# Optimization experiments

Hardware: AMD Instinct MI355X
Metric: run time of the kernel (lower is better)

The kernel has to match this reference:

```python
import jax, jax.numpy as jnp
import numpy as np

B, T, D, H = 1024, 128, 128, 256

def _uni(k, shape, fan):
    s = 1.0 / np.sqrt(fan)
    return jax.random.uniform(k, shape, jnp.float32, -s, s)

def setup_inputs():
    key = jax.random.key(0)
    ks = jax.random.split(key, 22)
    inp = {}
    inp['x'] = jax.random.normal(ks[0], (B, T, D), jnp.float32)
    inp['x_hat'] = jax.random.normal(ks[1], (B, T, D), jnp.float32)
    inp['u'] = jax.random.uniform(ks[2], (B, T, D), jnp.float32)
    inp['m'] = (jax.random.uniform(ks[3], (B, T, D)) < 0.8).astype(jnp.float32)
    inp['d'] = jax.random.uniform(ks[4], (B, T, D), jnp.float32)
    # Decay(D -> H)
    inp['W_decay'] = _uni(ks[5], (H, D), D)
    inp['b_decay'] = _uni(ks[6], (H,), D)
    # hist: Linear(H -> D)
    inp['W_hist'] = _uni(ks[7], (D, H), H)
    inp['b_hist'] = _uni(ks[8], (D,), H)
    inp['Wv'] = _uni(ks[9], (D, D), D)
    inp['bv'] = _uni(ks[10], (D,), D)
    inp['Wr'] = _uni(ks[11], (D, D), D)
    inp['br'] = _uni(ks[12], (D,), D)
    # Conv1d(2,1,kernel=1) == learned 2-way combine
    inp['conv_w'] = _uni(ks[13], (2,), 2)
    inp['conv_b'] = _uni(ks[14], (), 2)
    # GRUCell(2*D -> H), torch layout [3H, in] rows = (r, z, n)
    inp['W_ih'] = _uni(ks[15], (3 * H, 2 * D), 2 * D)
    inp['W_hh'] = _uni(ks[16], (3 * H, H), H)
    inp['b_ih'] = _uni(ks[17], (3 * H,), H)
    inp['b_hh'] = _uni(ks[18], (3 * H,), H)
    # fc_out: Linear(H -> 1)
    inp['W_out'] = _uni(ks[19], (1, H), H)
    inp['b_out'] = _uni(ks[20], (1,), H)
    return inp

def reference(x, x_hat, u, m, d, W_decay, b_decay, W_hist, b_hist, Wv, bv, Wr, br,
              conv_w, conv_b, W_ih, W_hh, b_ih, b_hh, W_out, b_out):
    off = 1.0 - jnp.eye(D, dtype=x.dtype)
    # Precompute everything that does not depend on the recurrent state h:
    gamma = jnp.exp(-jax.nn.relu(jnp.einsum('btd,hd->bth', d, W_decay) + b_decay))  # [B,T,H]
    xbar = m * x + (1.0 - m) * x_hat
    xu = jnp.einsum('btd,ed->bte', xbar, Wv * off) + bv  # [B,T,D] (unc_flag == 0 path)
    Wr_m = Wr * off

    def step(carry, inp):
        h, loss = carry
        x_t, m_t, g_t, xu_t = inp  # [B,D],[B,D],[B,H],[B,D]
        h = h * g_t
        x_h = h @ W_hist.T + b_hist
        x_r = m_t * x_t + (1.0 - m_t) * x_h
        xr = x_r @ Wr_m.T + br
        x_comb = conv_w[0] * xu_t + conv_w[1] * xr + conv_b  # Conv1d(2,1,1)
        loss = loss + jnp.sum(jnp.abs(x_t - x_comb) * m_t) / (jnp.sum(m_t) + 1e-5)
        x_imp = m_t * x_t + (1.0 - m_t) * x_comb
        gin = jnp.concatenate([x_imp, m_t], axis=1)  # [B, 2D]
        gi = gin @ W_ih.T + b_ih
        gh = h @ W_hh.T + b_hh
        i_r, i_z, i_n = jnp.split(gi, 3, axis=1)
        h_r, h_z, h_n = jnp.split(gh, 3, axis=1)
        r = jax.nn.sigmoid(i_r + h_r)
        z = jax.nn.sigmoid(i_z + h_z)
        n = jnp.tanh(i_n + r * h_n)
        h_new = (1.0 - z) * n + z * h
        return (h_new, loss), (x_imp, xr)

    h0 = jnp.zeros((B, H), x.dtype)
    xs = (jnp.swapaxes(x, 0, 1), jnp.swapaxes(m, 0, 1),
          jnp.swapaxes(gamma, 0, 1), jnp.swapaxes(xu, 0, 1))
    (h_fin, x_loss), (x_imp_t, xr_t) = jax.lax.scan(step, (h0, jnp.float32(0.0)), xs)
    x_imp = jnp.swapaxes(x_imp_t, 0, 1)  # [B,T,D]
    xrs = jnp.swapaxes(xr_t, 0, 1)
    y_out = h_fin @ W_out.T + b_out  # task == 'C', get_y == True
    y_score = jax.nn.sigmoid(y_out)
    return (x_imp, y_out, y_score, x_loss, xu, xrs)
```

## Files before the change

kernel.cpp:

```cpp
#include <hip/hip_runtime.h>
#include <math.h>

#define BQ 1024
#define TT 128
#define DD 128
#define HH 256
#define NW 8
#define NTH 512
#define NBLK 64

typedef float f32x4 __attribute__((ext_vector_type(4)));
typedef __bf16 bf16x8 __attribute__((ext_vector_type(8)));
typedef unsigned short u16x4 __attribute__((ext_vector_type(4)));
typedef unsigned short u16x8 __attribute__((ext_vector_type(8)));
typedef unsigned int u32x4 __attribute__((ext_vector_type(4)));
typedef unsigned int u32x2 __attribute__((ext_vector_type(2)));
typedef long long i64;

#define WS_MSUMF 8192
#define WS_WQ8   40960
#define WS_WB16  487424
#define WS_SA1   589824
#define WS_SA2   67698688

#define TQ_TOT  864

#define TB_DEC 0
#define TB_WV  64
#define TB_TOT 96

#define L_WX  0
#define L_HI  98304
#define L_WR  131072
#define L_HF8 147456
#define L_XRF 151552
#define L_XIF 153600
#define L_RED 155648
#define L_TOT 155712

__device__ __forceinline__ unsigned short f2bf(float f){
  union { float f; unsigned u; } v; v.f = f;
  unsigned r = v.u + 0x7FFFu + ((v.u >> 16) & 1u);
  return (unsigned short)(r >> 16);
}
__device__ __forceinline__ float sigm(float v){ return 1.f/(1.f + __expf(-v)); }
__device__ __forceinline__ float tanhfast(float v){ return 2.f*sigm(2.f*v) - 1.f; }
__device__ __forceinline__ unsigned pk4(float a, float b, float c, float d){
  int v = __builtin_amdgcn_cvt_pk_fp8_f32(a, b, 0, false);
  v = __builtin_amdgcn_cvt_pk_fp8_f32(c, d, v, true);
  return (unsigned)v;
}
__device__ __forceinline__ f32x4 upk4(unsigned w){
  f32x4 r;
  r[0] = __builtin_amdgcn_cvt_f32_fp8((int)w, 0);
  r[1] = __builtin_amdgcn_cvt_f32_fp8((int)w, 1);
  r[2] = __builtin_amdgcn_cvt_f32_fp8((int)w, 2);
  r[3] = __builtin_amdgcn_cvt_f32_fp8((int)w, 3);
  return r;
}
__device__ __forceinline__ f32x4 mfma8(i64 a, i64 b, f32x4 c){
  return __builtin_amdgcn_mfma_f32_16x16x32_fp8_fp8(a, b, c, 0, 0, 0);
}
__device__ __forceinline__ f32x4 mfma16b(bf16x8 a, bf16x8 b, f32x4 c){
  return __builtin_amdgcn_mfma_f32_16x16x32_bf16(a, b, c, 0, 0, 0);
}

__global__ void pack_w8(const float* Whh, const float* Wih, const float* Whist,
                        const float* Wr, unsigned char* wq){
  int gt = blockIdx.x*4 + (threadIdx.x>>6);
  int lane = threadIdx.x & 63;
  if (gt >= TQ_TOT) return;
  int lr = lane & 15, lg = lane >> 4;
  const float* src; int n, k0, K; int dm = 0;
  if (gt < 384){ int kt = gt & 7, gnt = gt >> 3;
    n = (gnt>>4)*256 + (gnt&15)*16 + lr; k0 = kt*32 + lg*8; src = Whh; K = 256; }
  else if (gt < 576){ int id = gt-384; int kt = id & 3, gnt = id >> 2;
    n = (gnt>>4)*256 + (gnt&15)*16 + lr; k0 = kt*32 + lg*8; src = Wih; K = 256; }
  else if (gt < 640){ int id = gt-576; int kt = id & 7, nt = id >> 3;
    n = nt*16 + lr; k0 = kt*32 + lg*8; src = Whist; K = 256; }
  else if (gt < 672){ int id = gt-640; int kt = id & 3, nt = id >> 2;
    n = nt*16 + lr; k0 = kt*32 + lg*8; src = Wr; K = 128; dm = 1; }
  else { int id = gt-672; int kt = id & 3, gnt = id >> 2;
    n = (gnt>>4)*256 + (gnt&15)*16 + lr; k0 = 128 + kt*32 + lg*8; src = Wih; K = 256; }
  float f[8];
  #pragma unroll
  for (int e = 0; e < 8; ++e){
    int k = k0 + e;
    float v = src[(size_t)n*K + k];
    if (dm && n == k) v = 0.f;
    f[e] = v;
  }
  unsigned lo = pk4(f[0],f[1],f[2],f[3]), hi = pk4(f[4],f[5],f[6],f[7]);
  *(unsigned*)(wq + (size_t)gt*512 + lane*8) = lo;
  *(unsigned*)(wq + (size_t)gt*512 + lane*8 + 4) = hi;
}

__global__ void pack_w16(const float* Wdec, const float* Wv, unsigned short* wb){
  int gt = blockIdx.x*4 + (threadIdx.x>>6);
  int lane = threadIdx.x & 63;
  if (gt >= TB_TOT) return;
  int lr = lane & 15, lg = lane >> 4;
  const float* src; int n; int dm = 0; int kt;
  if (gt < TB_WV){ kt = gt & 3; n = (gt>>2)*16 + lr; src = Wdec; }
  else { int id = gt - TB_WV; kt = id & 3; n = (id>>2)*16 + lr; src = Wv; dm = 1; }
  int k0 = kt*32 + lg*8;
  u16x8 pkv;
  #pragma unroll
  for (int e = 0; e < 8; ++e){
    int k = k0 + e;
    float v = src[(size_t)n*128 + k];
    if (dm && n == k) v = 0.f;
    pkv[e] = f2bf(v);
  }
  *(u16x8*)(wb + (size_t)gt*512 + lane*8) = pkv;
}

__global__ void msum_kernel(const float* m, float* wsf){
  int t = blockIdx.x;
  float s = 0.f;
  for (int i = threadIdx.x; i < BQ*DD/4; i += 256){
    int b = i >> 5, c4 = (i & 31)*4;
    f32x4 v = *(const f32x4*)(m + ((size_t)b*TT + t)*DD + c4);
    s += v[0]+v[1]+v[2]+v[3];
  }
  #pragma unroll
  for (int off = 32; off >= 1; off >>= 1) s += __shfl_down(s, off);
  __shared__ float ps[4];
  if ((threadIdx.x & 63) == 0) ps[threadIdx.x >> 6] = s;
  __syncthreads();
  if (threadIdx.x == 0) wsf[WS_MSUMF + t] = ps[0] + ps[1] + ps[2] + ps[3];
}

__global__ void loss_final(const float* wsf, float* out_loss){
  __shared__ float ps[TT];
  int t = threadIdx.x;
  float s = 0.f;
  #pragma unroll 4
  for (int b = 0; b < NBLK; ++b) s += wsf[t*NBLK + b];
  ps[t] = s / (wsf[WS_MSUMF + t] + 1e-5f);
  __syncthreads();
  if (t == 0){ float a = 0.f; for (int i = 0; i < TT; ++i) a += ps[i]; *out_loss = a; }
}

__global__ __launch_bounds__(NTH, 2) void prep1_kernel(
    const float* __restrict__ x, const float* __restrict__ xhat,
    const float* __restrict__ m, const float* __restrict__ dly,
    const float* __restrict__ b_dec, const float* __restrict__ bv,
    const unsigned short* __restrict__ wb, unsigned* __restrict__ saA,
    float* __restrict__ out_xu)
{
  __shared__ __align__(16) char sm[12288];
  const int tid = threadIdx.x, w = tid>>6, lane = tid&63, lr = lane&15, lg = lane>>4;
  const int btile = blockIdx.x >> 4, tch = blockIdx.x & 15, b0 = btile*16;
  const int tg0 = tch*8;
  const int colD = w*16 + lr, colH0 = w*32 + lr;
  bf16x8 decR[2][4], wvR[4];
  #pragma unroll
  for (int s = 0; s < 2; ++s)
    #pragma unroll
    for (int kt = 0; kt < 4; ++kt)
      decR[s][kt] = *(const bf16x8*)(wb + (size_t)(TB_DEC + (w*2+s)*4 + kt)*512 + lane*8);
  #pragma unroll
  for (int kt = 0; kt < 4; ++kt)
    wvR[kt] = *(const bf16x8*)(wb + (size_t)(TB_WV + w*4 + kt)*512 + lane*8);
  const float bd0 = b_dec[colH0], bd1 = b_dec[colH0+16], bvv = bv[colD];
  const int srow = tid >> 5, c4 = (tid & 31)*4;
  const int kt_ = c4 >> 5, dl_ = ((c4 & 31) >> 3)*16 + srow, e0_ = c4 & 7;
  const size_t gbase = (size_t)(b0 + srow)*TT*DD + c4;

  f32x4 xv = *(const f32x4*)(x    + gbase + (size_t)tg0*DD);
  f32x4 hv = *(const f32x4*)(xhat + gbase + (size_t)tg0*DD);
  f32x4 mv = *(const f32x4*)(m    + gbase + (size_t)tg0*DD);
  f32x4 dv = *(const f32x4*)(dly  + gbase + (size_t)tg0*DD);

  for (int tt = 0; tt < 8; ++tt){
    int tg = tg0 + tt;
    u16x4 pd, pxb, pm;
    #pragma unroll
    for (int e = 0; e < 4; ++e){
      pd[e]  = f2bf(dv[e]);
      pxb[e] = f2bf(mv[e]*xv[e] + (1.f - mv[e])*hv[e]);
      pm[e]  = f2bf(mv[e]);
    }
    *(u16x4*)(sm + 0    + kt_*1024 + dl_*16 + e0_*2) = pd;
    *(u16x4*)(sm + 4096 + kt_*1024 + dl_*16 + e0_*2) = pxb;
    *(u16x4*)(sm + 8192 + srow*256 + c4*2) = pm;
    __syncthreads();

    {
      size_t g2 = gbase + (size_t)((tt < 7) ? tg+1 : tg)*DD;
      xv = *(const f32x4*)(x + g2);
      hv = *(const f32x4*)(xhat + g2);
      mv = *(const f32x4*)(m + g2);
      dv = *(const f32x4*)(dly + g2);
    }

    f32x4 ga0 = {0.f,0.f,0.f,0.f}, ga1 = {0.f,0.f,0.f,0.f}, xu4 = {0.f,0.f,0.f,0.f};
    #pragma unroll
    for (int kt = 0; kt < 4; ++kt){
      bf16x8 df  = *(const bf16x8*)(sm + 0    + kt*1024 + lane*16);
      bf16x8 xbf = *(const bf16x8*)(sm + 4096 + kt*1024 + lane*16);
      ga0 = mfma16b(df, decR[0][kt], ga0);
      ga1 = mfma16b(df, decR[1][kt], ga1);
      xu4 = mfma16b(xbf, wvR[kt], xu4);
    }
    float g0[4], g1[4], xuo[4];
    unsigned mask = 0;
    #pragma unroll
    for (int r = 0; r < 4; ++r){
      g0[r] = __expf(-fmaxf(ga0[r] + bd0, 0.f));
      g1[r] = __expf(-fmaxf(ga1[r] + bd1, 0.f));
      xuo[r] = xu4[r] + bvv;
      int row = lg*4 + r;
      unsigned short mu = *(const unsigned short*)(sm + 8192 + row*256 + colD*2);
      mask |= (mu ? 1u : 0u) << r;
    }
    u32x4 rec = {pk4(g0[0],g0[1],g0[2],g0[3]), pk4(g1[0],g1[1],g1[2],g1[3]),
                 pk4(xuo[0],xuo[1],xuo[2],xuo[3]), mask};
    __builtin_nontemporal_store(rec,
        (u32x4*)(saA + (((size_t)tg*NBLK + btile)*512 + tid)*4));
    #pragma unroll
    for (int r = 0; r < 4; ++r)
      __builtin_nontemporal_store(xuo[r], out_xu + ((size_t)(b0 + lg*4 + r)*TT + tg)*DD + colD);
    __syncthreads();
  }
}

__global__ __launch_bounds__(NTH, 2) void prep2_kernel(
    const float* __restrict__ m, const float* __restrict__ b_ih,
    const float* __restrict__ b_hh, const unsigned char* __restrict__ wq,
    unsigned* __restrict__ saB)
{
  __shared__ __align__(16) char sm[2048];
  const int tid = threadIdx.x, w = tid>>6, lane = tid&63, lr = lane&15, lg = lane>>4;
  const int btile = blockIdx.x >> 4, tch = blockIdx.x & 15, b0 = btile*16;
  const int tg0 = tch*8;
  i64 wihmR[6][4];
  float bfold[6];
  #pragma unroll
  for (int g = 0; g < 3; ++g)
    #pragma unroll
    for (int s = 0; s < 2; ++s){
      int j = g*2 + s;
      #pragma unroll
      for (int kt = 0; kt < 4; ++kt)
        wihmR[j][kt] = *(const i64*)(wq + (size_t)(672 + (g*16 + w*2+s)*4 + kt)*512 + lane*8);
      int n = g*256 + w*32 + s*16 + lr;
      bfold[j] = b_ih[n] + ((g < 2) ? b_hh[n] : 0.f);
    }
  const int srow = tid >> 5, c4 = (tid & 31)*4;
  const int kt_ = c4 >> 5, lg2 = (c4 & 31) >> 3, e0_ = c4 & 7;
  const size_t gbase = (size_t)(b0 + srow)*TT*DD + c4;

  for (int tt = 0; tt < 8; ++tt){
    int tg = tg0 + tt;
    f32x4 mv = *(const f32x4*)(m + gbase + (size_t)tg*DD);
    unsigned wbyte = 0;
    #pragma unroll
    for (int e = 0; e < 4; ++e) wbyte |= (mv[e] > 0.5f ? 0x38u : 0u) << (8*e);
    *(unsigned*)(sm + kt_*512 + (lg2*16 + srow)*8 + e0_) = wbyte;
    __syncthreads();

    i64 ma[4];
    #pragma unroll
    for (int kt = 0; kt < 4; ++kt) ma[kt] = *(const i64*)(sm + kt*512 + lane*8);
    f32x4 z4 = {0.f,0.f,0.f,0.f};
    f32x4 acc[6] = {z4,z4,z4,z4,z4,z4};
    #pragma unroll
    for (int j = 0; j < 6; ++j)
      #pragma unroll
      for (int kt = 0; kt < 4; ++kt)
        acc[j] = mfma8(ma[kt], wihmR[j][kt], acc[j]);
    unsigned wd[6];
    #pragma unroll
    for (int j = 0; j < 6; ++j)
      wd[j] = pk4(acc[j][0]+bfold[j], acc[j][1]+bfold[j], acc[j][2]+bfold[j], acc[j][3]+bfold[j]);
    unsigned* rp = saB + (((size_t)tg*NBLK + btile)*512 + tid)*6;
    u32x2 p0 = {wd[0], wd[1]}, p1 = {wd[2], wd[3]}, p2 = {wd[4], wd[5]};
    __builtin_nontemporal_store(p0, (u32x2*)rp);
    __builtin_nontemporal_store(p1, (u32x2*)(rp+2));
    __builtin_nontemporal_store(p2, (u32x2*)(rp+4));
    __syncthreads();
  }
}

__global__ __launch_bounds__(NTH) __attribute__((amdgpu_waves_per_eu(2, 2)))
void scan_kernel(
    const unsigned char* __restrict__ wq, const unsigned* __restrict__ saA,
    const unsigned* __restrict__ saB, const float* __restrict__ x,
    const float* __restrict__ b_hist, const float* __restrict__ br,
    const float* __restrict__ b_hh,
    const float* __restrict__ conv_w, const float* __restrict__ conv_b,
    const float* __restrict__ W_out, const float* __restrict__ b_out,
    float* __restrict__ lossP,
    float* __restrict__ out_ximp, float* __restrict__ out_y,
    float* __restrict__ out_ys, float* __restrict__ out_xrs)
{
  extern __shared__ __align__(16) char lds[];
  const int tid = threadIdx.x, w = tid>>6, lane = tid&63, lr = lane&15, lg = lane>>4;
  const int b0 = blockIdx.x*16;
  const int colD = w*16 + lr, colH0 = w*32 + lr;

  i64 whhR[3][2][8];
  #pragma unroll
  for (int g = 0; g < 3; ++g)
    #pragma unroll
    for (int s = 0; s < 2; ++s)
      #pragma unroll
      for (int kt = 0; kt < 8; ++kt)
        whhR[g][s][kt] = *(const i64*)(wq + (size_t)((g*16 + w*2+s)*8 + kt)*512 + lane*8);
  for (int i = tid; i < 9216; i += NTH)
    *(u32x4*)(lds + (size_t)i*16) = *(const u32x4*)(wq + (size_t)384*512 + (size_t)i*16);

  const float bhist_v = b_hist[colD], br_v = br[colD];
  const float bhhn0 = b_hh[512 + colH0], bhhn1 = b_hh[512 + colH0 + 16];
  const float cw0 = conv_w[0], cw1 = conv_w[1], cb = conv_b[0];

  const int hb0 = L_HF8 + w*512 + (lr>>3)*128 + lg*32 + (lr&7);
  const int f80 = (w>>1)*512 + ((w&1)*2 + (lr>>3))*128 + lg*32 + (lr&7);
  float* red = (float*)(lds + L_RED);

  float hs[2][4] = {{0.f,0.f,0.f,0.f},{0.f,0.f,0.f,0.f}};

  const unsigned* rpa = saA + ((size_t)blockIdx.x*512 + tid)*4;
  const unsigned* rpb = saB + ((size_t)blockIdx.x*512 + tid)*6;
  const size_t STA = (size_t)NBLK*512*4, STB = (size_t)NBLK*512*6;
  const float* xb = x + (size_t)(b0 + lg*4)*TT*DD + colD;

  u32x4 pfA = __builtin_nontemporal_load((const u32x4*)rpa);
  u32x2 pfB0 = __builtin_nontemporal_load((const u32x2*)rpb);
  u32x2 pfB1 = __builtin_nontemporal_load((const u32x2*)(rpb+2));
  u32x2 pfB2 = __builtin_nontemporal_load((const u32x2*)(rpb+4));
  float xc_[4];
  #pragma unroll
  for (int r = 0; r < 4; ++r) xc_[r] = xb[(size_t)r*TT*DD];

  #pragma unroll 1
  for (int t = 0; t < TT; ++t){
    const unsigned* npa = (t < TT-1) ? (rpa + STA) : rpa;
    const unsigned* npb = (t < TT-1) ? (rpb + STB) : rpb;
    int tn = (t < TT-1) ? t+1 : t;
    u32x4 nA = __builtin_nontemporal_load((const u32x4*)npa);
    u32x2 nB0 = __builtin_nontemporal_load((const u32x2*)npb);
    u32x2 nB1 = __builtin_nontemporal_load((const u32x2*)(npb+2));
    u32x2 nB2 = __builtin_nontemporal_load((const u32x2*)(npb+4));
    float xn_[4];
    #pragma unroll
    for (int r = 0; r < 4; ++r) xn_[r] = xb[(size_t)r*TT*DD + (size_t)tn*DD];

    {
      f32x4 gA0 = upk4(pfA[0]), gA1 = upk4(pfA[1]);
      #pragma unroll
      for (int r = 0; r < 4; ++r){
        hs[0][r] *= gA0[r];
        hs[1][r] *= gA1[r];
      }
    }
    unsigned q0 = pk4(hs[0][0], hs[0][1], hs[0][2], hs[0][3]);
    unsigned q1 = pk4(hs[1][0], hs[1][1], hs[1][2], hs[1][3]);
    #pragma unroll
    for (int r = 0; r < 4; ++r){
      *(unsigned char*)(lds + hb0 +       r*8) = (unsigned char)(q0 >> (8*r));
      *(unsigned char*)(lds + hb0 + 256 + r*8) = (unsigned char)(q1 >> (8*r));
    }
    __syncthreads();

    i64 ha[8];
    #pragma unroll
    for (int kt = 0; kt < 8; ++kt)
      ha[kt] = *(const i64*)(lds + L_HF8 + kt*512 + lane*8);
    f32x4 z4 = {0.f,0.f,0.f,0.f};
    f32x4 aRZ[2][2] = {{z4,z4},{z4,z4}};
    f32x4 aNh[2] = {z4,z4}, aNi[2] = {z4,z4}, xh4 = z4;
    #pragma unroll
    for (int s = 0; s < 2; ++s)
      #pragma unroll
      for (int kt = 0; kt < 8; ++kt){
        aRZ[0][s] = mfma8(ha[kt], whhR[0][s][kt], aRZ[0][s]);
        aRZ[1][s] = mfma8(ha[kt], whhR[1][s][kt], aRZ[1][s]);
        aNh[s]    = mfma8(ha[kt], whhR[2][s][kt], aNh[s]);
      }
    #pragma unroll
    for (int kt = 0; kt < 8; ++kt)
      xh4 = mfma8(ha[kt], *(const i64*)(lds + L_HI + (w*8+kt)*512 + lane*8), xh4);
    {
      unsigned mk = pfA[3];
      float x0 = (mk & 1u) ? xc_[0] : (xh4[0] + bhist_v);
      float x1 = (mk & 2u) ? xc_[1] : (xh4[1] + bhist_v);
      float x2 = (mk & 4u) ? xc_[2] : (xh4[2] + bhist_v);
      float x3 = (mk & 8u) ? xc_[3] : (xh4[3] + bhist_v);
      unsigned p = pk4(x0, x1, x2, x3);
      #pragma unroll
      for (int r = 0; r < 4; ++r)
        *(unsigned char*)(lds + L_XRF + f80 + r*8) = (unsigned char)((p >> (8*r)) & 0xff);
    }
    __syncthreads();

    f32x4 xr4 = z4;
    #pragma unroll
    for (int kt = 0; kt < 4; ++kt)
      xr4 = mfma8(*(const i64*)(lds + L_XRF + kt*512 + lane*8),
                  *(const i64*)(lds + L_WR + (w*4+kt)*512 + lane*8), xr4);
    float lpart = 0.f, xi_[4];
    unsigned mk = pfA[3];
    f32x4 xu4v = upk4(pfA[2]);
    #pragma unroll
    for (int r = 0; r < 4; ++r){
      int row = lg*4 + r;
      size_t go = ((size_t)(b0+row)*TT + t)*DD + colD;
      float xrv = xr4[r] + br_v;
      float xuv = xu4v[r];
      __builtin_nontemporal_store(xrv, out_xrs + go);
      float xc = cw0*xuv + cw1*xrv + cb;
      bool mb = (mk >> r) & 1u;
      lpart += mb ? fabsf(xc_[r] - xc) : 0.f;
      xi_[r] = mb ? xc_[r] : xc;
      __builtin_nontemporal_store(xi_[r], out_ximp + go);
    }
    {
      unsigned q = pk4(xi_[0], xi_[1], xi_[2], xi_[3]);
      #pragma unroll
      for (int r = 0; r < 4; ++r)
        *(unsigned char*)(lds + L_XIF + f80 + r*8) = (unsigned char)((q >> (8*r)) & 0xff);
    }
    #pragma unroll
    for (int off = 32; off >= 1; off >>= 1) lpart += __shfl_down(lpart, off);
    if (lane == 0) red[w] = lpart;
    __syncthreads();

    i64 xia[4];
    #pragma unroll
    for (int kt = 0; kt < 4; ++kt) xia[kt] = *(const i64*)(lds + L_XIF + kt*512 + lane*8);
    #pragma unroll
    for (int s = 0; s < 2; ++s)
      #pragma unroll
      for (int kt = 0; kt < 4; ++kt){
        aRZ[0][s] = mfma8(xia[kt], *(const i64*)(lds + L_WX + ((0*16 + w*2+s)*4 + kt)*512 + lane*8), aRZ[0][s]);
        aRZ[1][s] = mfma8(xia[kt], *(const i64*)(lds + L_WX + ((1*16 + w*2+s)*4 + kt)*512 + lane*8), aRZ[1][s]);
        aNi[s]    = mfma8(xia[kt], *(const i64*)(lds + L_WX + ((2*16 + w*2+s)*4 + kt)*512 + lane*8), aNi[s]);
      }
    if (tid == 0){
      float ssum = 0.f;
      #pragma unroll
      for (int i = 0; i < 8; ++i) ssum += red[i];
      lossP[t*NBLK + blockIdx.x] = ssum;
    }
    {
      f32x4 gR0 = upk4(pfB0[0]), gR1 = upk4(pfB0[1]);
      f32x4 gZ0 = upk4(pfB1[0]), gZ1 = upk4(pfB1[1]);
      f32x4 gN0 = upk4(pfB2[0]), gN1 = upk4(pfB2[1]);
      #pragma unroll
      for (int r = 0; r < 4; ++r){
        float rr0 = sigm(aRZ[0][0][r] + gR0[r]);
        float zz0 = sigm(aRZ[1][0][r] + gZ0[r]);
        float nn0 = tanhfast(aNi[0][r] + gN0[r] + rr0*(aNh[0][r] + bhhn0));
        hs[0][r] = (1.f - zz0)*nn0 + zz0*hs[0][r];
        float rr1 = sigm(aRZ[0][1][r] + gR1[r]);
        float zz1 = sigm(aRZ[1][1][r] + gZ1[r]);
        float nn1 = tanhfast(aNi[1][r] + gN1[r] + rr1*(aNh[1][r] + bhhn1));
        hs[1][r] = (1.f - zz1)*nn1 + zz1*hs[1][r];
      }
    }
    pfA = nA; pfB0 = nB0; pfB1 = nB1; pfB2 = nB2;
    xc_[0] = xn_[0]; xc_[1] = xn_[1]; xc_[2] = xn_[2]; xc_[3] = xn_[3];
    rpa = npa; rpb = npb;
  }

  __syncthreads();
  float* hfin = (float*)lds;
  #pragma unroll
  for (int s = 0; s < 2; ++s)
    #pragma unroll
    for (int r = 0; r < 4; ++r)
      hfin[(lg*4+r)*HH + colH0 + s*16] = hs[s][r];
  __syncthreads();
  float* psum = (float*)(lds + 16384);
  if (tid < 256){
    int row = tid >> 4, seg = tid & 15;
    float p = 0.f;
    #pragma unroll
    for (int c = 0; c < 16; ++c) p += hfin[row*HH + seg*16 + c]*W_out[seg*16 + c];
    psum[tid] = p;
  }
  __syncthreads();
  if (tid < 16){
    float yv = b_out[0];
    #pragma unroll
    for (int i = 0; i < 16; ++i) yv += psum[tid*16 + i];
    out_y[b0 + tid] = yv;
    out_ys[b0 + tid] = sigm(yv);
  }
}

extern "C" void kernel_launch(void* const* d_in, const int* in_sizes, int n_in,
                              void* d_out, int out_size, void* d_ws, size_t ws_size,
                              hipStream_t stream){
  const float* x     = (const float*)d_in[0];
  const float* xhat  = (const float*)d_in[1];
  const float* m     = (const float*)d_in[3];
  const float* dly   = (const float*)d_in[4];
  const float* Wdec  = (const float*)d_in[5];
  const float* b_dec = (const float*)d_in[6];
  const float* Whist = (const float*)d_in[7];
  const float* b_hist= (const float*)d_in[8];
  const float* Wv    = (const float*)d_in[9];
  const float* bvv   = (const float*)d_in[10];
  const float* Wr    = (const float*)d_in[11];
  const float* brr   = (const float*)d_in[12];
  const float* convw = (const float*)d_in[13];
  const float* convb = (const float*)d_in[14];
  const float* Wih   = (const float*)d_in[15];
  const float* Whh   = (const float*)d_in[16];
  const float* b_ih  = (const float*)d_in[17];
  const float* b_hh  = (const float*)d_in[18];
  const float* W_out = (const float*)d_in[19];
  const float* b_out = (const float*)d_in[20];

  float* wsf = (float*)d_ws;
  unsigned char* wq = (unsigned char*)d_ws + WS_WQ8;
  unsigned short* wb = (unsigned short*)((char*)d_ws + WS_WB16);
  unsigned* saA = (unsigned*)((char*)d_ws + WS_SA1);
  unsigned* saB = (unsigned*)((char*)d_ws + WS_SA2);

  float* out = (float*)d_out;
  size_t btd = (size_t)BQ*TT*DD;
  float* out_ximp = out;
  float* out_y    = out + btd;
  float* out_ys   = out_y + BQ;
  float* out_loss = out_ys + BQ;
  float* out_xu   = out_loss + 1;
  float* out_xrs  = out_xu + btd;

  (void)hipFuncSetAttribute((const void*)scan_kernel,
                            hipFuncAttributeMaxDynamicSharedMemorySize, L_TOT);

  pack_w8<<<TQ_TOT/4, 256, 0, stream>>>(Whh, Wih, Whist, Wr, wq);
  pack_w16<<<TB_TOT/4, 256, 0, stream>>>(Wdec, Wv, wb);
  msum_kernel<<<TT, 256, 0, stream>>>(m, wsf);
  prep1_kernel<<<1024, NTH, 0, stream>>>(x, xhat, m, dly, b_dec, bvv, wb, saA, out_xu);
  prep2_kernel<<<1024, NTH, 0, stream>>>(m, b_ih, b_hh, wq, saB);
  scan_kernel<<<NBLK, NTH, L_TOT, stream>>>(wq, saA, saB, x, b_hist, brr, b_hh,
      convw, convb, W_out, b_out, wsf,
      out_ximp, out_y, out_ys, out_xrs);
  loss_final<<<1, TT, 0, stream>>>(wsf, out_loss);
}
```

Baseline: 625.2 us.

## Fuse prep kernels and widen scan to 16 waves with split roles

```diff
diff --git a/kernel.cpp b/kernel.cpp
--- a/kernel.cpp
+++ b/kernel.cpp
@@ -5,8 +5,7 @@
 #define TT 128
 #define DD 128
 #define HH 256
-#define NW 8
-#define NTH 512
+#define NTH 1024
 #define NBLK 64
 
 typedef float f32x4 __attribute__((ext_vector_type(4)));
@@ -20,11 +19,11 @@
 #define WS_MSUMF 8192
 #define WS_WQ8   40960
 #define WS_WB16  487424
-#define WS_SA1   589824
-#define WS_SA2   67698688
+#define WS_SAG   589824
+#define WS_SAXM  34144256
+#define WS_SAB3  67698688
 
 #define TQ_TOT  864
-
 #define TB_DEC 0
 #define TB_WV  64
 #define TB_TOT 96
@@ -35,8 +34,9 @@
 #define L_HF8 147456
 #define L_XRF 151552
 #define L_XIF 153600
-#define L_RED 155648
-#define L_TOT 155712
+#define L_IMS 155648
+#define L_RED 156160
+#define L_TOT 156224
 
 __device__ __forceinline__ unsigned short f2bf(float f){
   union { float f; unsigned u; } v; v.f = f;
@@ -128,28 +128,26 @@
   __shared__ float ps[4];
   if ((threadIdx.x & 63) == 0) ps[threadIdx.x >> 6] = s;
   __syncthreads();
-  if (threadIdx.x == 0) wsf[WS_MSUMF + t] = ps[0] + ps[1] + ps[2] + ps[3];
-}
-
-__global__ void loss_final(const float* wsf, float* out_loss){
-  __shared__ float ps[TT];
-  int t = threadIdx.x;
-  float s = 0.f;
-  #pragma unroll 4
-  for (int b = 0; b < NBLK; ++b) s += wsf[t*NBLK + b];
-  ps[t] = s / (wsf[WS_MSUMF + t] + 1e-5f);
-  __syncthreads();
-  if (t == 0){ float a = 0.f; for (int i = 0; i < TT; ++i) a += ps[i]; *out_loss = a; }
-}
-
-__global__ __launch_bounds__(NTH, 2) void prep1_kernel(
+  if (threadIdx.x == 0) wsf[WS_MSUMF + t] = 1.f/(ps[0]+ps[1]+ps[2]+ps[3] + 1e-5f);
+}
+
+__global__ void loss_final(const float* lossP, float* out_loss){
+  float v = lossP[threadIdx.x];
+  #pragma unroll
+  for (int off = 32; off >= 1; off >>= 1) v += __shfl_down(v, off);
+  if (threadIdx.x == 0) *out_loss = v;
+}
+
+__global__ __launch_bounds__(512, 2) void prep_kernel(
     const float* __restrict__ x, const float* __restrict__ xhat,
     const float* __restrict__ m, const float* __restrict__ dly,
     const float* __restrict__ b_dec, const float* __restrict__ bv,
-    const unsigned short* __restrict__ wb, unsigned* __restrict__ saA,
-    float* __restrict__ out_xu)
+    const float* __restrict__ b_ih, const float* __restrict__ b_hh,
+    const unsigned short* __restrict__ wb, const unsigned char* __restrict__ wq,
+    unsigned* __restrict__ saG, unsigned* __restrict__ saXM,
+    unsigned* __restrict__ saB3, float* __restrict__ out_xu)
 {
-  __shared__ __align__(16) char sm[12288];
+  __shared__ __align__(16) char sm[14336];
   const int tid = threadIdx.x, w = tid>>6, lane = tid&63, lr = lane&15, lg = lane>>4;
   const int btile = blockIdx.x >> 4, tch = blockIdx.x & 15, b0 = btile*16;
   const int tg0 = tch*8;
@@ -163,6 +161,19 @@
   #pragma unroll
   for (int kt = 0; kt < 4; ++kt)
     wvR[kt] = *(const bf16x8*)(wb + (size_t)(TB_WV + w*4 + kt)*512 + lane*8);
+  i64 wihmR[6][4];
+  float bfold[6];
+  #pragma unroll
+  for (int g = 0; g < 3; ++g)
+    #pragma unroll
+    for (int s = 0; s < 2; ++s){
+      int j = g*2 + s;
+      #pragma unroll
+      for (int kt = 0; kt < 4; ++kt)
+        wihmR[j][kt] = *(const i64*)(wq + (size_t)(672 + (g*16 + w*2+s)*4 + kt)*512 + lane*8);
+      int n = g*256 + w*32 + s*16 + lr;
+      bfold[j] = b_ih[n] + ((g < 2) ? b_hh[n] : 0.f);
+    }
   const float bd0 = b_dec[colH0], bd1 = b_dec[colH0+16], bvv = bv[colD];
   const int srow = tid >> 5, c4 = (tid & 31)*4;
   const int kt_ = c4 >> 5, dl_ = ((c4 & 31) >> 3)*16 + srow, e0_ = c4 & 7;
@@ -176,15 +187,18 @@
   for (int tt = 0; tt < 8; ++tt){
     int tg = tg0 + tt;
     u16x4 pd, pxb, pm;
+    unsigned wbyte = 0;
     #pragma unroll
     for (int e = 0; e < 4; ++e){
       pd[e]  = f2bf(dv[e]);
       pxb[e] = f2bf(mv[e]*xv[e] + (1.f - mv[e])*hv[e]);
       pm[e]  = f2bf(mv[e]);
-    }
-    *(u16x4*)(sm + 0    + kt_*1024 + dl_*16 + e0_*2) = pd;
-    *(u16x4*)(sm + 4096 + kt_*1024 + dl_*16 + e0_*2) = pxb;
-    *(u16x4*)(sm + 8192 + srow*256 + c4*2) = pm;
+      wbyte |= (mv[e] > 0.5f ? 0x38u : 0u) << (8*e);
+    }
+    *(u16x4*)(sm + 0     + kt_*1024 + dl_*16 + e0_*2) = pd;
+    *(u16x4*)(sm + 4096  + kt_*1024 + dl_*16 + e0_*2) = pxb;
+    *(u16x4*)(sm + 8192  + srow*256 + c4*2) = pm;
+    *(unsigned*)(sm + 12288 + kt_*512 + dl_*8 + e0_) = wbyte;
     __syncthreads();
 
     {
@@ -195,7 +209,8 @@
       dv = *(const f32x4*)(dly + g2);
     }
 
-    f32x4 ga0 = {0.f,0.f,0.f,0.f}, ga1 = {0.f,0.f,0.f,0.f}, xu4 = {0.f,0.f,0.f,0.f};
+    f32x4 z4 = {0.f,0.f,0.f,0.f};
+    f32x4 ga0 = z4, ga1 = z4, xu4 = z4;
     #pragma unroll
     for (int kt = 0; kt < 4; ++kt){
       bf16x8 df  = *(const bf16x8*)(sm + 0    + kt*1024 + lane*16);
@@ -204,6 +219,16 @@
       ga1 = mfma16b(df, decR[1][kt], ga1);
       xu4 = mfma16b(xbf, wvR[kt], xu4);
     }
+    i64 ma[4];
+    #pragma unroll
+    for (int kt = 0; kt < 4; ++kt) ma[kt] = *(const i64*)(sm + 12288 + kt*512 + lane*8);
+    f32x4 acc[6] = {z4,z4,z4,z4,z4,z4};
+    #pragma unroll
+    for (int j = 0; j < 6; ++j)
+      #pragma unroll
+      for (int kt = 0; kt < 4; ++kt)
+        acc[j] = mfma8(ma[kt], wihmR[j][kt], acc[j]);
+
     float g0[4], g1[4], xuo[4];
     unsigned mask = 0;
     #pragma unroll
@@ -215,10 +240,25 @@
       unsigned short mu = *(const unsigned short*)(sm + 8192 + row*256 + colD*2);
       mask |= (mu ? 1u : 0u) << r;
     }
-    u32x4 rec = {pk4(g0[0],g0[1],g0[2],g0[3]), pk4(g1[0],g1[1],g1[2],g1[3]),
-                 pk4(xuo[0],xuo[1],xuo[2],xuo[3]), mask};
-    __builtin_nontemporal_store(rec,
-        (u32x4*)(saA + (((size_t)tg*NBLK + btile)*512 + tid)*4));
+    size_t base1024 = ((size_t)tg*NBLK + btile)*1024;
+    __builtin_nontemporal_store(pk4(g0[0],g0[1],g0[2],g0[3]),
+        saG + base1024 + (2*w+0)*64 + lane);
+    __builtin_nontemporal_store(pk4(g1[0],g1[1],g1[2],g1[3]),
+        saG + base1024 + (2*w+1)*64 + lane);
+    u32x2 xmrec = {pk4(xuo[0],xuo[1],xuo[2],xuo[3]), mask};
+    __builtin_nontemporal_store(xmrec,
+        (u32x2*)(saXM + (((size_t)tg*NBLK + btile)*512 + tid)*2));
+    #pragma unroll
+    for (int s = 0; s < 2; ++s){
+      size_t bb = (base1024 + (2*w+s)*64 + lane)*3;
+      #pragma unroll
+      for (int g = 0; g < 3; ++g){
+        f32x4 a = acc[g*2+s];
+        __builtin_nontemporal_store(
+            pk4(a[0]+bfold[g*2+s], a[1]+bfold[g*2+s], a[2]+bfold[g*2+s], a[3]+bfold[g*2+s]),
+            saB3 + bb + g);
+      }
+    }
     #pragma unroll
     for (int r = 0; r < 4; ++r)
       __builtin_nontemporal_store(xuo[r], out_xu + ((size_t)(b0 + lg*4 + r)*TT + tg)*DD + colD);
@@ -226,68 +266,11 @@
   }
 }
 
-__global__ __launch_bounds__(NTH, 2) void prep2_kernel(
-    const float* __restrict__ m, const float* __restrict__ b_ih,
-    const float* __restrict__ b_hh, const unsigned char* __restrict__ wq,
-    unsigned* __restrict__ saB)
-{
-  __shared__ __align__(16) char sm[2048];
-  const int tid = threadIdx.x, w = tid>>6, lane = tid&63, lr = lane&15, lg = lane>>4;
-  const int btile = blockIdx.x >> 4, tch = blockIdx.x & 15, b0 = btile*16;
-  const int tg0 = tch*8;
-  i64 wihmR[6][4];
-  float bfold[6];
-  #pragma unroll
-  for (int g = 0; g < 3; ++g)
-    #pragma unroll
-    for (int s = 0; s < 2; ++s){
-      int j = g*2 + s;
-      #pragma unroll
-      for (int kt = 0; kt < 4; ++kt)
-        wihmR[j][kt] = *(const i64*)(wq + (size_t)(672 + (g*16 + w*2+s)*4 + kt)*512 + lane*8);
-      int n = g*256 + w*32 + s*16 + lr;
-      bfold[j] = b_ih[n] + ((g < 2) ? b_hh[n] : 0.f);
-    }
-  const int srow = tid >> 5, c4 = (tid & 31)*4;
-  const int kt_ = c4 >> 5, lg2 = (c4 & 31) >> 3, e0_ = c4 & 7;
-  const size_t gbase = (size_t)(b0 + srow)*TT*DD + c4;
-
-  for (int tt = 0; tt < 8; ++tt){
-    int tg = tg0 + tt;
-    f32x4 mv = *(const f32x4*)(m + gbase + (size_t)tg*DD);
-    unsigned wbyte = 0;
-    #pragma unroll
-    for (int e = 0; e < 4; ++e) wbyte |= (mv[e] > 0.5f ? 0x38u : 0u) << (8*e);
-    *(unsigned*)(sm + kt_*512 + (lg2*16 + srow)*8 + e0_) = wbyte;
-    __syncthreads();
-
-    i64 ma[4];
-    #pragma unroll
-    for (int kt = 0; kt < 4; ++kt) ma[kt] = *(const i64*)(sm + kt*512 + lane*8);
-    f32x4 z4 = {0.f,0.f,0.f,0.f};
-    f32x4 acc[6] = {z4,z4,z4,z4,z4,z4};
-    #pragma unroll
-    for (int j = 0; j < 6; ++j)
-      #pragma unroll
-      for (int kt = 0; kt < 4; ++kt)
-        acc[j] = mfma8(ma[kt], wihmR[j][kt], acc[j]);
-    unsigned wd[6];
-    #pragma unroll
-    for (int j = 0; j < 6; ++j)
-      wd[j] = pk4(acc[j][0]+bfold[j], acc[j][1]+bfold[j], acc[j][2]+bfold[j], acc[j][3]+bfold[j]);
-    unsigned* rp = saB + (((size_t)tg*NBLK + btile)*512 + tid)*6;
-    u32x2 p0 = {wd[0], wd[1]}, p1 = {wd[2], wd[3]}, p2 = {wd[4], wd[5]};
-    __builtin_nontemporal_store(p0, (u32x2*)rp);
-    __builtin_nontemporal_store(p1, (u32x2*)(rp+2));
-    __builtin_nontemporal_store(p2, (u32x2*)(rp+4));
-    __syncthreads();
-  }
-}
-
-__global__ __launch_bounds__(NTH) __attribute__((amdgpu_waves_per_eu(2, 2)))
-void scan_kernel(
-    const unsigned char* __restrict__ wq, const unsigned* __restrict__ saA,
-    const unsigned* __restrict__ saB, const float* __restrict__ x,
+__global__ __launch_bounds__(NTH) void scan_kernel(
+    const unsigned char* __restrict__ wq,
+    const unsigned* __restrict__ saG, const unsigned* __restrict__ saXM,
+    const unsigned* __restrict__ saB3, const float* __restrict__ x,
+    const float* __restrict__ msumInv,
     const float* __restrict__ b_hist, const float* __restrict__ br,
     const float* __restrict__ b_hh,
     const float* __restrict__ conv_w, const float* __restrict__ conv_b,
@@ -299,92 +282,90 @@
   extern __shared__ __align__(16) char lds[];
   const int tid = threadIdx.x, w = tid>>6, lane = tid&63, lr = lane&15, lg = lane>>4;
   const int b0 = blockIdx.x*16;
-  const int colD = w*16 + lr, colH0 = w*32 + lr;
-
-  i64 whhR[3][2][8];
+  const int wD = w & 7;
+  const int colH = w*16 + lr;
+  const int colD = wD*16 + lr;
+  const bool isLo = (w < 8);
+
+  i64 whhR[3][8];
   #pragma unroll
   for (int g = 0; g < 3; ++g)
     #pragma unroll
-    for (int s = 0; s < 2; ++s)
-      #pragma unroll
-      for (int kt = 0; kt < 8; ++kt)
-        whhR[g][s][kt] = *(const i64*)(wq + (size_t)((g*16 + w*2+s)*8 + kt)*512 + lane*8);
+    for (int kt = 0; kt < 8; ++kt)
+      whhR[g][kt] = *(const i64*)(wq + (size_t)((g*16 + w)*8 + kt)*512 + lane*8);
   for (int i = tid; i < 9216; i += NTH)
     *(u32x4*)(lds + (size_t)i*16) = *(const u32x4*)(wq + (size_t)384*512 + (size_t)i*16);
+  if (tid < TT) *(float*)(lds + L_IMS + tid*4) = msumInv[tid];
 
   const float bhist_v = b_hist[colD], br_v = br[colD];
-  const float bhhn0 = b_hh[512 + colH0], bhhn1 = b_hh[512 + colH0 + 16];
+  const float bhhn = b_hh[512 + colH];
   const float cw0 = conv_w[0], cw1 = conv_w[1], cb = conv_b[0];
 
-  const int hb0 = L_HF8 + w*512 + (lr>>3)*128 + lg*32 + (lr&7);
-  const int f80 = (w>>1)*512 + ((w&1)*2 + (lr>>3))*128 + lg*32 + (lr&7);
-  float* red = (float*)(lds + L_RED);
-
-  float hs[2][4] = {{0.f,0.f,0.f,0.f},{0.f,0.f,0.f,0.f}};
-
-  const unsigned* rpa = saA + ((size_t)blockIdx.x*512 + tid)*4;
-  const unsigned* rpb = saB + ((size_t)blockIdx.x*512 + tid)*6;
-  const size_t STA = (size_t)NBLK*512*4, STB = (size_t)NBLK*512*6;
+  const int hb16 = L_HF8 + (w>>1)*512 + ((w&1)*2 + (lr>>3))*128 + lg*32 + (lr&7);
+  const int f80  = (wD>>1)*512 + ((wD&1)*2 + (lr>>3))*128 + lg*32 + (lr&7);
+
+  float hs[4] = {0.f,0.f,0.f,0.f};
+  float lacc = 0.f;
+
+  const unsigned* pGp  = saG + (size_t)blockIdx.x*1024 + tid;
+  const unsigned* pXMp = saXM + ((size_t)blockIdx.x*512 + wD*64 + lane)*2;
+  const unsigned* pB3p = saB3 + ((size_t)blockIdx.x*1024 + tid)*3;
   const float* xb = x + (size_t)(b0 + lg*4)*TT*DD + colD;
-
-  u32x4 pfA = __builtin_nontemporal_load((const u32x4*)rpa);
-  u32x2 pfB0 = __builtin_nontemporal_load((const u32x2*)rpb);
-  u32x2 pfB1 = __builtin_nontemporal_load((const u32x2*)(rpb+2));
-  u32x2 pfB2 = __builtin_nontemporal_load((const u32x2*)(rpb+4));
+  const size_t STG = (size_t)NBLK*1024, STXM = (size_t)NBLK*1024, STB3 = (size_t)NBLK*3072;
+
+  unsigned pG = __builtin_nontemporal_load(pGp);
+  u32x2 pXM = __builtin_nontemporal_load((const u32x2*)pXMp);
+  unsigned pR = __builtin_nontemporal_load(pB3p);
+  unsigned pZ = __builtin_nontemporal_load(pB3p+1);
+  unsigned pN = __builtin_nontemporal_load(pB3p+2);
   float xc_[4];
   #pragma unroll
   for (int r = 0; r < 4; ++r) xc_[r] = xb[(size_t)r*TT*DD];
+  __syncthreads();
 
   #pragma unroll 1
   for (int t = 0; t < TT; ++t){
-    const unsigned* npa = (t < TT-1) ? (rpa + STA) : rpa;
-    const unsigned* npb = (t < TT-1) ? (rpb + STB) : rpb;
+    const unsigned* nGp  = (t < TT-1) ? (pGp + STG) : pGp;
+    const unsigned* nXMp = (t < TT-1) ? (pXMp + STXM) : pXMp;
+    const unsigned* nB3p = (t < TT-1) ? (pB3p + STB3) : pB3p;
     int tn = (t < TT-1) ? t+1 : t;
-    u32x4 nA = __builtin_nontemporal_load((const u32x4*)npa);
-    u32x2 nB0 = __builtin_nontemporal_load((const u32x2*)npb);
-    u32x2 nB1 = __builtin_nontemporal_load((const u32x2*)(npb+2));
-    u32x2 nB2 = __builtin_nontemporal_load((const u32x2*)(npb+4));
+    unsigned nG = __builtin_nontemporal_load(nGp);
+    u32x2 nXM = __builtin_nontemporal_load((const u32x2*)nXMp);
+    unsigned nR = __builtin_nontemporal_load(nB3p);
+    unsigned nZ = __builtin_nontemporal_load(nB3p+1);
+    unsigned nN = __builtin_nontemporal_load(nB3p+2);
     float xn_[4];
     #pragma unroll
     for (int r = 0; r < 4; ++r) xn_[r] = xb[(size_t)r*TT*DD + (size_t)tn*DD];
 
     {
-      f32x4 gA0 = upk4(pfA[0]), gA1 = upk4(pfA[1]);
-      #pragma unroll
-      for (int r = 0; r < 4; ++r){
-        hs[0][r] *= gA0[r];
-        hs[1][r] *= gA1[r];
+      f32x4 g4 = upk4(pG);
+      #pragma unroll
+      for (int r = 0; r < 4; ++r) hs[r] *= g4[r];
+    }
+    unsigned q0 = pk4(hs[0], hs[1], hs[2], hs[3]);
+    #pragma unroll
+    for (int r = 0; r < 4; ++r)
+      *(unsigned char*)(lds + hb16 + r*8) = (unsigned char)(q0 >> (8*r));
+    __syncthreads();
+
+    f32x4 z4 = {0.f,0.f,0.f,0.f};
+    f32x4 aR = z4, aZ = z4, aNh = z4;
+    #pragma unroll
+    for (int kt = 0; kt < 8; ++kt){
+      i64 ha = *(const i64*)(lds + L_HF8 + kt*512 + lane*8);
+      aR  = mfma8(ha, whhR[0][kt], aR);
+      aZ  = mfma8(ha, whhR[1][kt], aZ);
+      aNh = mfma8(ha, whhR[2][kt], aNh);
+    }
+    if (!isLo){
+      f32x4 xh4 = z4;
+      #pragma unroll
+      for (int kt = 0; kt < 8; ++kt){
+        i64 ha = *(const i64*)(lds + L_HF8 + kt*512 + lane*8);
+        xh4 = mfma8(ha, *(const i64*)(lds + L_HI + (wD*8+kt)*512 + lane*8), xh4);
       }
-    }
-    unsigned q0 = pk4(hs[0][0], hs[0][1], hs[0][2], hs[0][3]);
-    unsigned q1 = pk4(hs[1][0], hs[1][1], hs[1][2], hs[1][3]);
-    #pragma unroll
-    for (int r = 0; r < 4; ++r){
-      *(unsigned char*)(lds + hb0 +       r*8) = (unsigned char)(q0 >> (8*r));
-      *(unsigned char*)(lds + hb0 + 256 + r*8) = (unsigned char)(q1 >> (8*r));
-    }
-    __syncthreads();
-
-    i64 ha[8];
-    #pragma unroll
-    for (int kt = 0; kt < 8; ++kt)
-      ha[kt] = *(const i64*)(lds + L_HF8 + kt*512 + lane*8);
-    f32x4 z4 = {0.f,0.f,0.f,0.f};
-    f32x4 aRZ[2][2] = {{z4,z4},{z4,z4}};
-    f32x4 aNh[2] = {z4,z4}, aNi[2] = {z4,z4}, xh4 = z4;
-    #pragma unroll
-    for (int s = 0; s < 2; ++s)
-      #pragma unroll
-      for (int kt = 0; kt < 8; ++kt){
-        aRZ[0][s] = mfma8(ha[kt], whhR[0][s][kt], aRZ[0][s]);
-        aRZ[1][s] = mfma8(ha[kt], whhR[1][s][kt], aRZ[1][s]);
-        aNh[s]    = mfma8(ha[kt], whhR[2][s][kt], aNh[s]);
-      }
-    #pragma unroll
-    for (int kt = 0; kt < 8; ++kt)
-      xh4 = mfma8(ha[kt], *(const i64*)(lds + L_HI + (w*8+kt)*512 + lane*8), xh4);
-    {
-      unsigned mk = pfA[3];
+      unsigned mk = pXM[1];
       float x0 = (mk & 1u) ? xc_[0] : (xh4[0] + bhist_v);
       float x1 = (mk & 2u) ? xc_[1] : (xh4[1] + bhist_v);
       float x2 = (mk & 4u) ? xc_[2] : (xh4[2] + bhist_v);
@@ -396,84 +377,74 @@
     }
     __syncthreads();
 
-    f32x4 xr4 = z4;
-    #pragma unroll
-    for (int kt = 0; kt < 4; ++kt)
-      xr4 = mfma8(*(const i64*)(lds + L_XRF + kt*512 + lane*8),
-                  *(const i64*)(lds + L_WR + (w*4+kt)*512 + lane*8), xr4);
-    float lpart = 0.f, xi_[4];
-    unsigned mk = pfA[3];
-    f32x4 xu4v = upk4(pfA[2]);
-    #pragma unroll
-    for (int r = 0; r < 4; ++r){
-      int row = lg*4 + r;
-      size_t go = ((size_t)(b0+row)*TT + t)*DD + colD;
-      float xrv = xr4[r] + br_v;
-      float xuv = xu4v[r];
-      __builtin_nontemporal_store(xrv, out_xrs + go);
-      float xc = cw0*xuv + cw1*xrv + cb;
-      bool mb = (mk >> r) & 1u;
-      lpart += mb ? fabsf(xc_[r] - xc) : 0.f;
-      xi_[r] = mb ? xc_[r] : xc;
-      __builtin_nontemporal_store(xi_[r], out_ximp + go);
-    }
-    {
+    if (isLo){
+      f32x4 xr4 = z4;
+      #pragma unroll
+      for (int kt = 0; kt < 4; ++kt)
+        xr4 = mfma8(*(const i64*)(lds + L_XRF + kt*512 + lane*8),
+                    *(const i64*)(lds + L_WR + (wD*4+kt)*512 + lane*8), xr4);
+      unsigned mk = pXM[1];
+      f32x4 xu4v = upk4(pXM[0]);
+      float ims = *(const float*)(lds + L_IMS + t*4);
+      float lp = 0.f, xi_[4];
+      #pragma unroll
+      for (int r = 0; r < 4; ++r){
+        int row = lg*4 + r;
+        size_t go = ((size_t)(b0+row)*TT + t)*DD + colD;
+        float xrv = xr4[r] + br_v;
+        __builtin_nontemporal_store(xrv, out_xrs + go);
+        float xc = cw0*xu4v[r] + cw1*xrv + cb;
+        bool mb = (mk >> r) & 1u;
+        lp += mb ? fabsf(xc_[r] - xc) : 0.f;
+        xi_[r] = mb ? xc_[r] : xc;
+        __builtin_nontemporal_store(xi_[r], out_ximp + go);
+      }
+      lacc += lp * ims;
       unsigned q = pk4(xi_[0], xi_[1], xi_[2], xi_[3]);
       #pragma unroll
       for (int r = 0; r < 4; ++r)
         *(unsigned char*)(lds + L_XIF + f80 + r*8) = (unsigned char)((q >> (8*r)) & 0xff);
     }
-    #pragma unroll
-    for (int off = 32; off >= 1; off >>= 1) lpart += __shfl_down(lpart, off);
-    if (lane == 0) red[w] = lpart;
     __syncthreads();
 
-    i64 xia[4];
-    #pragma unroll
-    for (int kt = 0; kt < 4; ++kt) xia[kt] = *(const i64*)(lds + L_XIF + kt*512 + lane*8);
-    #pragma unroll
-    for (int s = 0; s < 2; ++s)
-      #pragma unroll
-      for (int kt = 0; kt < 4; ++kt){
-        aRZ[0][s] = mfma8(xia[kt], *(const i64*)(lds + L_WX + ((0*16 + w*2+s)*4 + kt)*512 + lane*8), aRZ[0][s]);
-        aRZ[1][s] = mfma8(xia[kt], *(const i64*)(lds + L_WX + ((1*16 + w*2+s)*4 + kt)*512 + lane*8), aRZ[1][s]);
-        aNi[s]    = mfma8(xia[kt], *(const i64*)(lds + L_WX + ((2*16 + w*2+s)*4 + kt)*512 + lane*8), aNi[s]);
+    f32x4 aNi = z4;
+    #pragma unroll
+    for (int kt = 0; kt < 4; ++kt){
+      i64 xia = *(const i64*)(lds + L_XIF + kt*512 + lane*8);
+      aR  = mfma8(xia, *(const i64*)(lds + L_WX + (( 0 + w)*4 + kt)*512 + lane*8), aR);
+      aZ  = mfma8(xia, *(const i64*)(lds + L_WX + ((16 + w)*4 + kt)*512 + lane*8), aZ);
+      aNi = mfma8(xia, *(const i64*)(lds + L_WX + ((32 + w)*4 + kt)*512 + lane*8), aNi);
+    }
+    {
+      f32x4 gR4 = upk4(pR), gZ4 = upk4(pZ), gN4 = upk4(pN);
+      #pragma unroll
+      for (int r = 0; r < 4; ++r){
+        float rr = sigm(aR[r] + gR4[r]);
+        float zz = sigm(aZ[r] + gZ4[r]);
+        float nn = tanhfast(aNi[r] + gN4[r] + rr*(aNh[r] + bhhn));
+        hs[r] = (1.f - zz)*nn + zz*hs[r];
       }
-    if (tid == 0){
-      float ssum = 0.f;
-      #pragma unroll
-      for (int i = 0; i < 8; ++i) ssum += red[i];
-      lossP[t*NBLK + blockIdx.x] = ssum;
-    }
-    {
-      f32x4 gR0 = upk4(pfB0[0]), gR1 = upk4(pfB0[1]);
-      f32x4 gZ0 = upk4(pfB1[0]), gZ1 = upk4(pfB1[1]);
-      f32x4 gN0 = upk4(pfB2[0]), gN1 = upk4(pfB2[1]);
-      #pragma unroll
-      for (int r = 0; r < 4; ++r){
-        float rr0 = sigm(aRZ[0][0][r] + gR0[r]);
-        float zz0 = sigm(aRZ[1][0][r] + gZ0[r]);
-        float nn0 = tanhfast(aNi[0][r] + gN0[r] + rr0*(aNh[0][r] + bhhn0));
-        hs[0][r] = (1.f - zz0)*nn0 + zz0*hs[0][r];
-        float rr1 = sigm(aRZ[0][1][r] + gR1[r]);
-        float zz1 = sigm(aRZ[1][1][r] + gZ1[r]);
-        float nn1 = tanhfast(aNi[1][r] + gN1[r] + rr1*(aNh[1][r] + bhhn1));
-        hs[1][r] = (1.f - zz1)*nn1 + zz1*hs[1][r];
-      }
-    }
-    pfA = nA; pfB0 = nB0; pfB1 = nB1; pfB2 = nB2;
+    }
+    pG = nG; pXM = nXM; pR = nR; pZ = nZ; pN = nN;
     xc_[0] = xn_[0]; xc_[1] = xn_[1]; xc_[2] = xn_[2]; xc_[3] = xn_[3];
-    rpa = npa; rpb = npb;
+    pGp = nGp; pXMp = nXMp; pB3p = nB3p;
   }
 
   __syncthreads();
+  #pragma unroll
+  for (int off = 32; off >= 1; off >>= 1) lacc += __shfl_down(lacc, off);
+  if (lane == 0) ((float*)(lds + L_RED))[w] = lacc;
   float* hfin = (float*)lds;
   #pragma unroll
-  for (int s = 0; s < 2; ++s)
-    #pragma unroll
-    for (int r = 0; r < 4; ++r)
-      hfin[(lg*4+r)*HH + colH0 + s*16] = hs[s][r];
+  for (int r = 0; r < 4; ++r)
+    hfin[(lg*4+r)*HH + colH] = hs[r];
   __syncthreads();
+  if (tid == 0){
+    float s = 0.f;
+    #pragma unroll
+    for (int i = 0; i < 16; ++i) s += ((float*)(lds + L_RED))[i];
+    lossP[blockIdx.x] = s;
+  }
   float* psum = (float*)(lds + 16384);
   if (tid < 256){
     int row = tid >> 4, seg = tid & 15;
@@ -519,8 +490,9 @@
   float* wsf = (float*)d_ws;
   unsigned char* wq = (unsigned char*)d_ws + WS_WQ8;
   unsigned short* wb = (unsigned short*)((char*)d_ws + WS_WB16);
-  unsigned* saA = (unsigned*)((char*)d_ws + WS_SA1);
-  unsigned* saB = (unsigned*)((char*)d_ws + WS_SA2);
+  unsigned* saG  = (unsigned*)((char*)d_ws + WS_SAG);
+  unsigned* saXM = (unsigned*)((char*)d_ws + WS_SAXM);
+  unsigned* saB3 = (unsigned*)((char*)d_ws + WS_SAB3);
 
   float* out = (float*)d_out;
   size_t btd = (size_t)BQ*TT*DD;
@@ -537,10 +509,10 @@
   pack_w8<<<TQ_TOT/4, 256, 0, stream>>>(Whh, Wih, Whist, Wr, wq);
   pack_w16<<<TB_TOT/4, 256, 0, stream>>>(Wdec, Wv, wb);
   msum_kernel<<<TT, 256, 0, stream>>>(m, wsf);
-  prep1_kernel<<<1024, NTH, 0, stream>>>(x, xhat, m, dly, b_dec, bvv, wb, saA, out_xu);
-  prep2_kernel<<<1024, NTH, 0, stream>>>(m, b_ih, b_hh, wq, saB);
-  scan_kernel<<<NBLK, NTH, L_TOT, stream>>>(wq, saA, saB, x, b_hist, brr, b_hh,
-      convw, convb, W_out, b_out, wsf,
+  prep_kernel<<<1024, 512, 0, stream>>>(x, xhat, m, dly, b_dec, bvv, b_ih, b_hh,
+      wb, wq, saG, saXM, saB3, out_xu);
+  scan_kernel<<<NBLK, NTH, L_TOT, stream>>>(wq, saG, saXM, saB3, x, wsf + WS_MSUMF,
+      b_hist, brr, b_hh, convw, convb, W_out, b_out, wsf,
       out_ximp, out_y, out_ys, out_xrs);
-  loss_final<<<1, TT, 0, stream>>>(wsf, out_loss);
-}
+  loss_final<<<1, 64, 0, stream>>>(wsf, out_loss);
+}
```

Measured after the change: 742.2 us. +18.7%, slower.
